# Kernel tuning notes

Measured on AMD Instinct MI355X. Metric: run time of the kernel, lower is better.

## Reference

```python
import jax, jax.numpy as jnp
import numpy as np

A = 20.0  # sigmoid sharpness used by the module

def norm_sigmoid(x):
    # module's sigmoid: min/max normalize over the whole tensor, then steep sigmoid
    xn = (x - jnp.min(x)) / (jnp.max(x) - jnp.min(x))
    return jax.nn.sigmoid(A * xn)

def setup_inputs() -> dict:
    key = jax.random.key(0)
    ks = jax.random.split(key, 10)
    B, T = 2048, 512
    input_dim, nh1, nh2, nh3, output_dim = 1, 256, 256, 128, 1
    def lin(k, fan_in, fan_out):
        bound = 1.0 / np.sqrt(fan_in)
        kw, kb = jax.random.split(k)
        W = jax.random.uniform(kw, (fan_out, fan_in), jnp.float32, -bound, bound)
        b = jax.random.uniform(kb, (fan_out,), jnp.float32, -bound, bound)
        return W, b
    W1, b1 = lin(ks[0], input_dim, nh1)
    W2, b2 = lin(ks[1], nh1, nh2)
    W4, b4 = lin(ks[2], nh3, output_dim)
    j_w = jax.random.normal(ks[3], (nh3,), jnp.float32)
    k_w = jax.random.normal(ks[4], (nh3,), jnp.float32)
    X = jax.random.normal(ks[5], (B, T), jnp.float32)
    return {"X": X, "W1": W1, "b1": b1, "W2": W2, "b2": b2,
            "W4": W4, "b4": b4, "j_w": j_w, "k_w": k_w}

def reference(X, W1, b1, W2, b2, W4, b4, j_w, k_w):
    B, T = X.shape
    nh3 = j_w.shape[0]
    xs = jnp.swapaxes(X, 0, 1)[:, :, None]  # [T, B, 1] scalar input per step

    def step(state, x_t):
        out1 = norm_sigmoid(x_t @ W1.T + b1)          # [B, nh1]
        out2 = norm_sigmoid(out1 @ W2.T + b2)         # [B, nh2]
        j, k = out2[:, :nh3], out2[:, nh3:]
        inp_j = norm_sigmoid(j * j_w)
        inp_k = norm_sigmoid(k * k_w)
        new_state = (1.0 - state) * inp_j + (1.0 - inp_k) * state  # flip-flop update
        out4 = norm_sigmoid(new_state @ W4.T + b4)    # [B, 1]
        return new_state, out4

    state0 = jnp.zeros((B, nh3), X.dtype)
    _, ys = jax.lax.scan(step, state0, xs)            # ys: [T, B, 1]
    return jnp.squeeze(jnp.swapaxes(ys, 0, 1), axis=2)  # [B, T]
```

## Files before the change

kernel.cpp:

```cpp
#include <hip/hip_runtime.h>

#define TT 512
#define BB 2048
#define HH 256

typedef _Float16 f16x8 __attribute__((ext_vector_type(8)));
typedef _Float16 f16x4 __attribute__((ext_vector_type(4)));
typedef float f32x4 __attribute__((ext_vector_type(4)));

__device__ __forceinline__ float sigf(float z) {
    return __builtin_amdgcn_rcpf(1.0f + __expf(-z));
}
__device__ __forceinline__ unsigned f2o(float f) {
    unsigned u = __float_as_uint(f);
    return (u & 0x80000000u) ? ~u : (u | 0x80000000u);
}
__device__ __forceinline__ float o2f(unsigned o) {
    unsigned u = (o & 0x80000000u) ? (o & 0x7fffffffu) : ~o;
    return __uint_as_float(u);
}

__global__ __launch_bounds__(256) void k0_stats(const float* __restrict__ X,
                                                const float* __restrict__ W1,
                                                const float* __restrict__ b1,
                                                float* __restrict__ mn1f, float* __restrict__ s1f,
                                                unsigned* __restrict__ colGmn,
                                                unsigned* __restrict__ colGmx,
                                                float2* __restrict__ statep) {
    int t = blockIdx.x, tid = threadIdx.x;
    statep[blockIdx.x * 256 + tid] = make_float2(0.f, 0.f);
    colGmn[(size_t)t * 256 + tid] = 0xFFFFFFFFu;
    colGmx[(size_t)t * 256 + tid] = 0u;
    __shared__ float rmn[256], rmx[256];
    float mn = 3.4e38f, mx = -3.4e38f;
    for (int b = tid; b < BB; b += 256) {
        float v = X[(size_t)b * TT + t];
        mn = fminf(mn, v); mx = fmaxf(mx, v);
    }
    rmn[tid] = mn; rmx[tid] = mx; __syncthreads();
    for (int s = 128; s > 0; s >>= 1) {
        if (tid < s) { rmn[tid] = fminf(rmn[tid], rmn[tid + s]); rmx[tid] = fmaxf(rmx[tid], rmx[tid + s]); }
        __syncthreads();
    }
    float xmn = rmn[0], xmx = rmx[0];
    __syncthreads();
    float w = W1[tid], bb = b1[tid];
    float v0 = w * xmn + bb, v1 = w * xmx + bb;
    rmn[tid] = fminf(v0, v1); rmx[tid] = fmaxf(v0, v1); __syncthreads();
    for (int s = 128; s > 0; s >>= 1) {
        if (tid < s) { rmn[tid] = fminf(rmn[tid], rmn[tid + s]); rmx[tid] = fmaxf(rmx[tid], rmx[tid + s]); }
        __syncthreads();
    }
    if (tid == 0) {
        mn1f[t] = rmn[0];
        s1f[t] = 20.0f / (rmx[0] - rmn[0]);
    }
}

__global__ __launch_bounds__(256) void k0b_cvt(const float* __restrict__ W2,
                                               _Float16* __restrict__ W2hi) {
    int i4 = (blockIdx.x * 256 + threadIdx.x) * 4;
    float4 v = *(const float4*)&W2[i4];
    f16x4 h;
    h[0] = (_Float16)v.x; h[1] = (_Float16)v.y; h[2] = (_Float16)v.z; h[3] = (_Float16)v.w;
    *(f16x4*)&W2hi[i4] = h;
}

__global__ __launch_bounds__(256) void k1_gemm(const float* __restrict__ X,
                                               const float* __restrict__ W1,
                                               const float* __restrict__ b1,
                                               const _Float16* __restrict__ W2h,
                                               const float* __restrict__ b2,
                                               const float* __restrict__ mn1f,
                                               const float* __restrict__ s1f,
                                               float* __restrict__ buf,
                                               unsigned* __restrict__ colGmn,
                                               unsigned* __restrict__ colGmx,
                                               int tbase) {
    int tl = blockIdx.z, t = tbase + tl;
    int bBase = blockIdx.x * 64;
    int tid = threadIdx.x;
    __shared__ __align__(16) char smem[33792];
    _Float16* A0 = (_Float16*)smem;
    _Float16* A1 = A0 + 8192;
    float* C_lds = (float*)smem;
    int lane = tid & 63, w = tid >> 6;
    int l15 = lane & 15, hi2 = lane >> 4;

    int sr = tid >> 2, ks0 = (tid & 3) * 32;
    float xr = X[(size_t)(bBase + sr) * TT + t];
    float mn1 = mn1f[t], s1 = s1f[t];

    const _Float16* bp[4];
#pragma unroll
    for (int j = 0; j < 4; ++j)
        bp[j] = W2h + (size_t)(w * 64 + j * 16 + l15) * HH + hi2 * 8;

    f32x4 acc[4][4];
#pragma unroll
    for (int i = 0; i < 4; ++i)
#pragma unroll
        for (int j = 0; j < 4; ++j) acc[i][j] = (f32x4)0.0f;

#pragma unroll
    for (int kh = 0; kh < 2; ++kh) {
        if (kh) __syncthreads();
#pragma unroll
        for (int g = 0; g < 4; ++g) {
            int klocal = ks0 + g * 8;
            int k = kh * 128 + klocal;
            float4 wa = *(const float4*)&W1[k];
            float4 wb = *(const float4*)&W1[k + 4];
            float4 ba = *(const float4*)&b1[k];
            float4 bb = *(const float4*)&b1[k + 4];
            float av[8];
            av[0] = sigf((xr * wa.x + ba.x - mn1) * s1);
            av[1] = sigf((xr * wa.y + ba.y - mn1) * s1);
            av[2] = sigf((xr * wa.z + ba.z - mn1) * s1);
            av[3] = sigf((xr * wa.w + ba.w - mn1) * s1);
            av[4] = sigf((xr * wb.x + bb.x - mn1) * s1);
            av[5] = sigf((xr * wb.y + bb.y - mn1) * s1);
            av[6] = sigf((xr * wb.z + bb.z - mn1) * s1);
            av[7] = sigf((xr * wb.w + bb.w - mn1) * s1);
            f16x8 hv, lv;
#pragma unroll
            for (int u = 0; u < 8; ++u) {
                _Float16 ah = (_Float16)av[u];
                hv[u] = ah;
                lv[u] = (_Float16)(av[u] - (float)ah);
            }
            int kgs = (klocal >> 3) ^ (sr & 7);
            *(f16x8*)&A0[sr * 128 + kgs * 8] = hv;
            *(f16x8*)&A1[sr * 128 + kgs * 8] = lv;
        }
        __syncthreads();
#pragma unroll
        for (int s = 0; s < 4; ++s) {
            f16x8 bh[4];
#pragma unroll
            for (int j = 0; j < 4; ++j) bh[j] = *(const f16x8*)(bp[j] + kh * 128 + s * 32);
#pragma unroll
            for (int i = 0; i < 4; ++i) {
                int row = i * 16 + l15;
                int kgs = (s * 4 + hi2) ^ (row & 7);
                f16x8 ah = *(const f16x8*)&A0[row * 128 + kgs * 8];
                f16x8 al = *(const f16x8*)&A1[row * 128 + kgs * 8];
#pragma unroll
                for (int j = 0; j < 4; ++j) {
                    acc[i][j] = __builtin_amdgcn_mfma_f32_16x16x32_f16(al, bh[j], acc[i][j], 0, 0, 0);
                    acc[i][j] = __builtin_amdgcn_mfma_f32_16x16x32_f16(ah, bh[j], acc[i][j], 0, 0, 0);
                }
            }
        }
    }

    float b2r[4];
#pragma unroll
    for (int j = 0; j < 4; ++j) b2r[j] = b2[w * 64 + j * 16 + l15];
#pragma unroll
    for (int j = 0; j < 4; ++j) {
        float vmn = 3.4e38f, vmx = -3.4e38f;
#pragma unroll
        for (int i = 0; i < 4; ++i)
#pragma unroll
            for (int q = 0; q < 4; ++q) {
                float v = acc[i][j][q] + b2r[j];
                acc[i][j][q] = v;
                vmn = fminf(vmn, v); vmx = fmaxf(vmx, v);
            }
        vmn = fminf(vmn, __shfl_xor(vmn, 16)); vmn = fminf(vmn, __shfl_xor(vmn, 32));
        vmx = fmaxf(vmx, __shfl_xor(vmx, 16)); vmx = fmaxf(vmx, __shfl_xor(vmx, 32));
        if (hi2 == 0) {
            int c = w * 64 + j * 16 + l15;
            atomicMin(&colGmn[(size_t)t * 256 + c], f2o(vmn));
            atomicMax(&colGmx[(size_t)t * 256 + c], f2o(vmx));
        }
    }

#pragma unroll
    for (int r = 0; r < 2; ++r) {
        __syncthreads();
        if ((w >> 1) == r) {
            int cl0 = (w & 1) * 64;
#pragma unroll
            for (int i = 0; i < 4; ++i)
#pragma unroll
                for (int j = 0; j < 4; ++j)
#pragma unroll
                    for (int q = 0; q < 4; ++q)
                        C_lds[(i * 16 + hi2 * 4 + q) * 132 + cl0 + j * 16 + l15] = acc[i][j][q];
        }
        __syncthreads();
#pragma unroll
        for (int it = 0; it < 8; ++it) {
            int idx = it * 256 + tid;
            int row = idx >> 5, c4 = idx & 31;
            float4 v = *(const float4*)&C_lds[row * 132 + c4 * 4];
            *(float4*)&buf[((size_t)tl * BB + bBase + row) * HH + r * 128 + c4 * 4] = v;
        }
    }
}

__global__ __launch_bounds__(256) void k1b(const unsigned* __restrict__ colGmn,
                                           const unsigned* __restrict__ colGmx,
                                           const float* __restrict__ j_w,
                                           const float* __restrict__ k_w,
                                           float* __restrict__ mn2f, float* __restrict__ s2f,
                                           float* __restrict__ mjf, float* __restrict__ sjf,
                                           float* __restrict__ mkf, float* __restrict__ skf,
                                           int tbase) {
    int t = tbase + blockIdx.x, tid = threadIdx.x;
    __shared__ float ra[256], rb[256];
    float cmn = o2f(colGmn[(size_t)t * 256 + tid]);
    float cmx = o2f(colGmx[(size_t)t * 256 + tid]);
    ra[tid] = cmn; rb[tid] = cmx; __syncthreads();
    for (int s = 128; s > 0; s >>= 1) {
        if (tid < s) { ra[tid] = fminf(ra[tid], ra[tid + s]); rb[tid] = fmaxf(rb[tid], rb[tid + s]); }
        __syncthreads();
    }
    float mn2 = ra[0], mx2 = rb[0];
    float s2 = 20.0f / (mx2 - mn2);
    __syncthreads();
    float wv = (tid < 128) ? j_w[tid] : k_w[tid - 128];
    float ea = sigf((cmn - mn2) * s2) * wv;
    float eb = sigf((cmx - mn2) * s2) * wv;
    ra[tid] = fminf(ea, eb); rb[tid] = fmaxf(ea, eb); __syncthreads();
    for (int s = 64; s > 0; s >>= 1) {
        if ((tid & 127) < s) { ra[tid] = fminf(ra[tid], ra[tid + s]); rb[tid] = fmaxf(rb[tid], rb[tid + s]); }
        __syncthreads();
    }
    if (tid == 0) {
        mn2f[t] = mn2; s2f[t] = s2;
        mjf[t] = ra[0]; sjf[t] = 20.0f / (rb[0] - ra[0]);
    }
    if (tid == 128) {
        mkf[t] = ra[128]; skf[t] = 20.0f / (rb[128] - ra[128]);
    }
}

__global__ __launch_bounds__(256) void k3_scan(const float* __restrict__ buf,
                                               const float* __restrict__ W4,
                                               const float* __restrict__ b4,
                                               const float* __restrict__ mn2f, const float* __restrict__ s2f,
                                               const float* __restrict__ mjf, const float* __restrict__ sjf,
                                               const float* __restrict__ mkf, const float* __restrict__ skf,
                                               const float* __restrict__ j_w, const float* __restrict__ k_w,
                                               float2* __restrict__ statep,
                                               float* __restrict__ out4p,
                                               int tbase, int TC) {
    __shared__ float n2L[512], c2L[512], mjL[512], sjL[512], mkL[512], skL[512];
    int tid = threadIdx.x;
    for (int tl = tid; tl < TC; tl += 256) {
        int t = tbase + tl;
        n2L[tl] = mn2f[t]; c2L[tl] = s2f[t];
        mjL[tl] = mjf[t]; sjL[tl] = sjf[t];
        mkL[tl] = mkf[t]; skL[tl] = skf[t];
    }
    __syncthreads();
    int wave = tid >> 6, lane = tid & 63;
    int b = blockIdx.x * 4 + wave;
    float w40 = W4[2 * lane], w41 = W4[2 * lane + 1];
    float jw0 = j_w[2 * lane], jw1 = j_w[2 * lane + 1];
    float kw0 = k_w[2 * lane], kw1 = k_w[2 * lane + 1];
    float bb4 = b4[0];
    float2 stv = statep[b * 64 + lane];
    float s0 = stv.x, s1v = stv.y;
    const float2* basep = (const float2*)buf;
    const int rowstride = BB * 128;
    int off0 = b * 128 + lane;
    float rsave = 0.f;
    float2 jq[8], kq[8];
#pragma unroll
    for (int u = 0; u < 8; ++u) {
        jq[u] = basep[(size_t)u * rowstride + off0];
        kq[u] = basep[(size_t)u * rowstride + off0 + 64];
    }
    for (int t0 = 0; t0 < TC; t0 += 8) {
#pragma unroll
        for (int u = 0; u < 8; ++u) {
            int tl = t0 + u;
            float2 jp = jq[u], kp = kq[u];
            int tn = tl + 8;
            if (tn < TC) {
                jq[u] = basep[(size_t)tn * rowstride + off0];
                kq[u] = basep[(size_t)tn * rowstride + off0 + 64];
            }
            float n2 = n2L[tl], c2 = c2L[tl];
            float pj0 = sigf((jp.x - n2) * c2) * jw0;
            float pj1 = sigf((jp.y - n2) * c2) * jw1;
            float pk0 = sigf((kp.x - n2) * c2) * kw0;
            float pk1 = sigf((kp.y - n2) * c2) * kw1;
            float ij0 = sigf((pj0 - mjL[tl]) * sjL[tl]);
            float ij1 = sigf((pj1 - mjL[tl]) * sjL[tl]);
            float ik0 = sigf((pk0 - mkL[tl]) * skL[tl]);
            float ik1 = sigf((pk1 - mkL[tl]) * skL[tl]);
            s0 = ij0 + s0 * (1.0f - ij0 - ik0);
            s1v = ij1 + s1v * (1.0f - ij1 - ik1);
            float r = s0 * w40 + s1v * w41;
#pragma unroll
            for (int m = 1; m < 64; m <<= 1) r += __shfl_xor(r, m);
            if (lane == (tl & 63)) rsave = r + bb4;
        }
        if (((t0 + 8) & 63) == 0) {
            int base = t0 + 8 - 64;
            out4p[(size_t)b * TT + tbase + base + lane] = rsave;
        }
    }
    if (TC < 64 && lane < TC) out4p[(size_t)b * TT + tbase + lane] = rsave;
    statep[b * 64 + lane] = make_float2(s0, s1v);
}

__global__ __launch_bounds__(256) void k3b(const float* __restrict__ out4p,
                                           float* __restrict__ mn4f, float* __restrict__ s4f) {
    int t = blockIdx.x, tid = threadIdx.x;
    __shared__ float rmn[256], rmx[256];
    float mn = 3.4e38f, mx = -3.4e38f;
    for (int b = tid; b < BB; b += 256) {
        float v = out4p[(size_t)b * TT + t];
        mn = fminf(mn, v); mx = fmaxf(mx, v);
    }
    rmn[tid] = mn; rmx[tid] = mx; __syncthreads();
    for (int s = 128; s > 0; s >>= 1) {
        if (tid < s) { rmn[tid] = fminf(rmn[tid], rmn[tid + s]); rmx[tid] = fmaxf(rmx[tid], rmx[tid + s]); }
        __syncthreads();
    }
    if (tid == 0) { mn4f[t] = rmn[0]; s4f[t] = 20.0f / (rmx[0] - rmn[0]); }
}

__global__ __launch_bounds__(256) void k4_final(float* __restrict__ out,
                                                const float* __restrict__ mn4f,
                                                const float* __restrict__ s4f) {
    int i = blockIdx.x * 256 + threadIdx.x;
    float4 v = ((const float4*)out)[i];
    int t0 = (i * 4) & (TT - 1);
    float4 mn = *(const float4*)&mn4f[t0];
    float4 sc = *(const float4*)&s4f[t0];
    float4 r;
    r.x = sigf((v.x - mn.x) * sc.x);
    r.y = sigf((v.y - mn.y) * sc.y);
    r.z = sigf((v.z - mn.z) * sc.z);
    r.w = sigf((v.w - mn.w) * sc.w);
    ((float4*)out)[i] = r;
}

extern "C" void kernel_launch(void* const* d_in, const int* in_sizes, int n_in,
                              void* d_out, int out_size, void* d_ws, size_t ws_size,
                              hipStream_t stream) {
    const float* X  = (const float*)d_in[0];
    const float* W1 = (const float*)d_in[1];
    const float* b1 = (const float*)d_in[2];
    const float* W2 = (const float*)d_in[3];
    const float* b2 = (const float*)d_in[4];
    const float* W4 = (const float*)d_in[5];
    const float* b4 = (const float*)d_in[6];
    const float* j_w = (const float*)d_in[7];
    const float* k_w = (const float*)d_in[8];
    float* out = (float*)d_out;

    const size_t stateB = (size_t)BB * 64 * sizeof(float2);
    const size_t colGB  = (size_t)TT * 256 * 2 * 4;
    const size_t w2hB   = (size_t)HH * HH * 2;
    const size_t statsB = 65536;
    int TC = 512;
    while (TC > 8 && ((size_t)TC * BB * HH * 4 + stateB + colGB + w2hB + statsB) > ws_size) TC >>= 1;
    int NC = TT / TC;

    char* w = (char*)d_ws;
    float* buf = (float*)w;
    size_t off = (size_t)TC * BB * HH * 4;
    float2* statep = (float2*)(w + off); off += stateB;
    unsigned* colGmn = (unsigned*)(w + off); off += colGB / 2;
    unsigned* colGmx = (unsigned*)(w + off); off += colGB / 2;
    _Float16* W2hi = (_Float16*)(w + off); off += w2hB;
    float* fst = (float*)(w + off);
    float* mn1f = fst;        float* s1f = fst + 512;
    float* mn2f = fst + 1024; float* s2f = fst + 1536;
    float* mjf  = fst + 2048; float* sjf = fst + 2560;
    float* mkf  = fst + 3072; float* skf = fst + 3584;
    float* mn4f = fst + 4096; float* s4f = fst + 4608;
    float* out4p = out;

    k0_stats<<<512, 256, 0, stream>>>(X, W1, b1, mn1f, s1f, colGmn, colGmx, statep);
    k0b_cvt<<<64, 256, 0, stream>>>(W2, W2hi);
    for (int c = 0; c < NC; ++c) {
        int tbase = c * TC;
        k1_gemm<<<dim3(BB / 64, 1, TC), 256, 0, stream>>>(X, W1, b1, W2hi, b2, mn1f, s1f,
                                                          buf, colGmn, colGmx, tbase);
        k1b<<<TC, 256, 0, stream>>>(colGmn, colGmx, j_w, k_w, mn2f, s2f, mjf, sjf, mkf, skf, tbase);
        k3_scan<<<512, 256, 0, stream>>>(buf, W4, b4, mn2f, s2f, mjf, sjf, mkf, skf,
                                         j_w, k_w, statep, out4p, tbase, TC);
    }
    k3b<<<512, 256, 0, stream>>>(out4p, mn4f, s4f);
    k4_final<<<1024, 256, 0, stream>>>(out, mn4f, s4f);
}
```

Before: 984.0 us.

## Store GEMM tiles in MFMA fragment layout and gather them in the recurrence

The GEMM epilogue now writes each accumulator fragment straight to global memory in native MFMA register order with nontemporal stores. This removes the LDS transpose stage and its two barriers. The recurrence kernel recomputes matching swizzled offsets and loads scalar values instead of contiguous float2 pairs. In exchange, the consumer's reads become strided scalar gathers, which may hurt coalescing in the step-serial loop.

After: 1.199 ms. +21.8%, slower.

```diff
diff --git a/kernel.cpp b/kernel.cpp
--- a/kernel.cpp
+++ b/kernel.cpp
@@ -80,10 +80,8 @@
     int tl = blockIdx.z, t = tbase + tl;
     int bBase = blockIdx.x * 64;
     int tid = threadIdx.x;
-    __shared__ __align__(16) char smem[33792];
-    _Float16* A0 = (_Float16*)smem;
-    _Float16* A1 = A0 + 8192;
-    float* C_lds = (float*)smem;
+    __shared__ __align__(16) _Float16 A0[64 * 128];
+    __shared__ __align__(16) _Float16 A1[64 * 128];
     int lane = tid & 63, w = tid >> 6;
     int l15 = lane & 15, hi2 = lane >> 4;
 
@@ -154,6 +152,7 @@
         }
     }
 
+    float* tileout = buf + (size_t)tl * (BB * HH) + (size_t)blockIdx.x * (64 * HH);
     float b2r[4];
 #pragma unroll
     for (int j = 0; j < 4; ++j) b2r[j] = b2[w * 64 + j * 16 + l15];
@@ -161,42 +160,23 @@
     for (int j = 0; j < 4; ++j) {
         float vmn = 3.4e38f, vmx = -3.4e38f;
 #pragma unroll
-        for (int i = 0; i < 4; ++i)
+        for (int i = 0; i < 4; ++i) {
+            f32x4 v;
 #pragma unroll
             for (int q = 0; q < 4; ++q) {
-                float v = acc[i][j][q] + b2r[j];
-                acc[i][j][q] = v;
-                vmn = fminf(vmn, v); vmx = fmaxf(vmx, v);
+                float x = acc[i][j][q] + b2r[j];
+                v[q] = x;
+                vmn = fminf(vmn, x); vmx = fmaxf(vmx, x);
             }
+            __builtin_nontemporal_store(v,
+                (f32x4*)&tileout[(size_t)((((w * 4 + j) * 4 + i) * 64 + lane) * 4)]);
+        }
         vmn = fminf(vmn, __shfl_xor(vmn, 16)); vmn = fminf(vmn, __shfl_xor(vmn, 32));
         vmx = fmaxf(vmx, __shfl_xor(vmx, 16)); vmx = fmaxf(vmx, __shfl_xor(vmx, 32));
         if (hi2 == 0) {
             int c = w * 64 + j * 16 + l15;
             atomicMin(&colGmn[(size_t)t * 256 + c], f2o(vmn));
             atomicMax(&colGmx[(size_t)t * 256 + c], f2o(vmx));
-        }
-    }
-
-#pragma unroll
-    for (int r = 0; r < 2; ++r) {
-        __syncthreads();
-        if ((w >> 1) == r) {
-            int cl0 = (w & 1) * 64;
-#pragma unroll
-            for (int i = 0; i < 4; ++i)
-#pragma unroll
-                for (int j = 0; j < 4; ++j)
-#pragma unroll
-                    for (int q = 0; q < 4; ++q)
-                        C_lds[(i * 16 + hi2 * 4 + q) * 132 + cl0 + j * 16 + l15] = acc[i][j][q];
-        }
-        __syncthreads();
-#pragma unroll
-        for (int it = 0; it < 8; ++it) {
-            int idx = it * 256 + tid;
-            int row = idx >> 5, c4 = idx & 31;
-            float4 v = *(const float4*)&C_lds[row * 132 + c4 * 4];
-            *(float4*)&buf[((size_t)tl * BB + bBase + row) * HH + r * 128 + c4 * 4] = v;
         }
     }
 }
@@ -265,31 +245,38 @@
     float bb4 = b4[0];
     float2 stv = statep[b * 64 + lane];
     float s0 = stv.x, s1v = stv.y;
-    const float2* basep = (const float2*)buf;
-    const int rowstride = BB * 128;
-    int off0 = b * 128 + lane;
+    int brow = b & 63;
+    int bi = brow >> 4, bhi2 = (brow >> 2) & 3, bq = brow & 3;
+    int offj0 = (((lane >> 5) * 4 + ((lane >> 3) & 3)) * 4 + bi) * 256 +
+                (bhi2 * 16 + 2 * (lane & 7)) * 4 + bq;
+    int offj1 = offj0 + 4;
+    int offk0 = offj0 + 8192, offk1 = offj1 + 8192;
+    const float* bp0 = buf + (size_t)(b >> 6) * 16384;
+    const size_t TSTR = (size_t)BB * HH;
     float rsave = 0.f;
-    float2 jq[8], kq[8];
+    float jq0[8], jq1[8], kq0[8], kq1[8];
 #pragma unroll
     for (int u = 0; u < 8; ++u) {
-        jq[u] = basep[(size_t)u * rowstride + off0];
-        kq[u] = basep[(size_t)u * rowstride + off0 + 64];
+        const float* p = bp0 + (size_t)u * TSTR;
+        jq0[u] = p[offj0]; jq1[u] = p[offj1];
+        kq0[u] = p[offk0]; kq1[u] = p[offk1];
     }
     for (int t0 = 0; t0 < TC; t0 += 8) {
 #pragma unroll
         for (int u = 0; u < 8; ++u) {
             int tl = t0 + u;
-            float2 jp = jq[u], kp = kq[u];
+            float jpx = jq0[u], jpy = jq1[u], kpx = kq0[u], kpy = kq1[u];
             int tn = tl + 8;
             if (tn < TC) {
-                jq[u] = basep[(size_t)tn * rowstride + off0];
-                kq[u] = basep[(size_t)tn * rowstride + off0 + 64];
+                const float* p = bp0 + (size_t)tn * TSTR;
+                jq0[u] = p[offj0]; jq1[u] = p[offj1];
+                kq0[u] = p[offk0]; kq1[u] = p[offk1];
             }
             float n2 = n2L[tl], c2 = c2L[tl];
-            float pj0 = sigf((jp.x - n2) * c2) * jw0;
-            float pj1 = sigf((jp.y - n2) * c2) * jw1;
-            float pk0 = sigf((kp.x - n2) * c2) * kw0;
-            float pk1 = sigf((kp.y - n2) * c2) * kw1;
+            float pj0 = sigf((jpx - n2) * c2) * jw0;
+            float pj1 = sigf((jpy - n2) * c2) * jw1;
+            float pk0 = sigf((kpx - n2) * c2) * kw0;
+            float pk1 = sigf((kpy - n2) * c2) * kw1;
             float ij0 = sigf((pj0 - mjL[tl]) * sjL[tl]);
             float ij1 = sigf((pj1 - mjL[tl]) * sjL[tl]);
             float ik0 = sigf((pk0 - mkL[tl]) * skL[tl]);
```
